# Optimization experiments

Measured on AMD Instinct MI355X. Metric: run time of the kernel, lower is better.

## Reference

```python
import jax, jax.numpy as jnp
import numpy as np

EPS = 1e-5

def conv(x, w, stride=1, pad=0, groups=1):
    # x: NCHW, w: OIHW
    return jax.lax.conv_general_dilated(
        x, w, window_strides=(stride, stride),
        padding=[(pad, pad), (pad, pad)],
        dimension_numbers=("NCHW", "OIHW", "NCHW"),
        feature_group_count=groups)

def bn_eval(x, gamma, beta, mean, var):
    scale = (gamma / jnp.sqrt(var + EPS))[None, :, None, None]
    shift = (beta - mean * gamma / jnp.sqrt(var + EPS))[None, :, None, None]
    return x * scale + shift

def setup_inputs() -> dict:
    key = jax.random.key(0)
    ks = jax.random.split(key, 12)
    B, Cin, H, W = 32, 64, 56, 56
    hidden, red, Cout, K = 384, 16, 64, 3
    f32 = jnp.float32
    x = jax.random.normal(ks[0], (B, Cin, H, W), dtype=f32)
    w_exp = jax.random.normal(ks[1], (hidden, Cin, 3, 3), dtype=f32) * 0.05
    w_dw  = jax.random.normal(ks[2], (hidden, 1, K, K), dtype=f32) * 0.1
    w_se1 = jax.random.normal(ks[3], (red, hidden, 1, 1), dtype=f32) * 0.05
    w_se2 = jax.random.normal(ks[4], (hidden, red, 1, 1), dtype=f32) * 0.1
    w_pw  = jax.random.normal(ks[5], (Cout, hidden, 1, 1), dtype=f32) * 0.05
    def bn_params(k, c):
        k1, k2 = jax.random.split(k)
        return (jnp.ones((c,), f32), jnp.zeros((c,), f32),
                jax.random.normal(k1, (c,), dtype=f32) * 0.01,
                jax.random.uniform(k2, (c,), dtype=f32, minval=0.5, maxval=1.5))
    g1, b1, m1, v1 = bn_params(ks[6], hidden)
    g2, b2, m2, v2 = bn_params(ks[7], hidden)
    g3, b3, m3, v3 = bn_params(ks[8], Cout)
    return dict(x=x, w_exp=w_exp, g1=g1, b1=b1, m1=m1, v1=v1,
                w_dw=w_dw, g2=g2, b2=b2, m2=m2, v2=v2,
                w_se1=w_se1, w_se2=w_se2, w_pw=w_pw,
                g3=g3, b3=b3, m3=m3, v3=v3)

def reference(x, w_exp, g1, b1, m1, v1, w_dw, g2, b2, m2, v2,
              w_se1, w_se2, w_pw, g3, b3, m3, v3):
    hidden = w_exp.shape[0]
    # expand conv (3x3) + BN + SiLU
    h = jax.nn.silu(bn_eval(conv(x, w_exp, stride=1, pad=1), g1, b1, m1, v1))
    # depthwise conv + BN + SiLU
    d = jax.nn.silu(bn_eval(conv(h, w_dw, stride=1, pad=1, groups=hidden), g2, b2, m2, v2))
    # squeeze-excitation: global avg pool -> 1x1 -> SiLU -> 1x1 -> sigmoid -> scale
    s = jnp.mean(d, axis=(2, 3), keepdims=True)            # [B, hidden, 1, 1]
    s = jax.nn.silu(conv(s, w_se1))
    s = jax.nn.sigmoid(conv(s, w_se2))
    d = d * s
    # pointwise projection + BN
    y = bn_eval(conv(d, w_pw), g3, b3, m3, v3)
    # eval mode: stochastic_depth is identity; quant_skip == (identity-quantized) input
    return y + x
```

## Files before the change

### kernel.cpp

```cpp
#include <hip/hip_runtime.h>

typedef unsigned short u16;
typedef unsigned int u32;
typedef __attribute__((ext_vector_type(2))) u32 u32x2;
typedef __attribute__((ext_vector_type(4))) u32 u32x4;
typedef __attribute__((ext_vector_type(4))) float f32x4;
typedef __attribute__((ext_vector_type(8))) short s16x8;

#define DEV __device__ __forceinline__

DEV float bflo(u32 u){ union{u32 i; float f;} c; c.i = u << 16; return c.f; }
DEV float bfhi(u32 u){ union{u32 i; float f;} c; c.i = u & 0xffff0000u; return c.f; }
DEV u16 f2b(float f){
  union{float f; u32 u;} c; c.f = f;
  u32 u = c.u;
  u32 r = (u + 0x7fffu + ((u >> 16) & 1u)) >> 16;
  return (u16)r;
}
DEV float fsilu(float v){ return v / (1.f + __expf(-v)); }

constexpr int Bn = 32, Cin = 64, H = 56, Wd = 56, HID = 384, CO = 64;
constexpr int HW = H * Wd;
constexpr float EPS = 1e-5f;

constexpr int XROW = 72 * 64;
constexpr int WTAP = 128 * 64;
constexpr int WOCT = 9 * WTAP;

__global__ __launch_bounds__(256) void k_prep_wbn(
    const float* __restrict__ w,
    const float* __restrict__ g1, const float* __restrict__ b1,
    const float* __restrict__ m1, const float* __restrict__ v1,
    const float* __restrict__ g3, const float* __restrict__ b3,
    const float* __restrict__ m3, const float* __restrict__ v3,
    u16* __restrict__ wt,
    float* __restrict__ sc1, float* __restrict__ sh1,
    float* __restrict__ sc3, float* __restrict__ sh3)
{
  const int blk = blockIdx.x;
  if (blk < 864) {
    int t = blk * 256 + threadIdx.x;
    int octile = t / WOCT, r = t - octile * WOCT;
    int tap = r / WTAP, r2 = r - tap * WTAP;
    int ocl = r2 >> 6, col = r2 & 63;
    int physo = col >> 3, j = col & 7;
    int olog = physo ^ (ocl & 7);
    int ic = olog * 8 + j;
    int oc = octile * 128 + ocl;
    wt[t] = f2b(w[(oc * Cin + ic) * 9 + tap]);
  } else {
    for (int t = threadIdx.x; t < HID; t += 256) {
      float sc = g1[t] * rsqrtf(v1[t] + EPS);
      sc1[t] = sc;
      sh1[t] = b1[t] - m1[t] * sc;
    }
    if (threadIdx.x < CO) {
      int t = threadIdx.x;
      float sc = g3[t] * rsqrtf(v3[t] + EPS);
      sc3[t] = sc;
      sh3[t] = b3[t] - m3[t] * sc;
    }
  }
}

__global__ __launch_bounds__(256, 2) void k_expand_mfma(
    const float* __restrict__ x, const u16* __restrict__ wt,
    const float* __restrict__ sc1, const float* __restrict__ sh1,
    u16* __restrict__ h, int b0)
{
  __shared__ u16 sB[4 * XROW];
  __shared__ u16 sA[2][WTAP];
  const int tid = threadIdx.x;
  const int ypair = blockIdx.x, b = blockIdx.y;
  const int gb = b0 + b;
  const int y0 = ypair * 2;
  const int wave = tid >> 6, ln = tid & 63;
  const int wm = wave >> 1, wn = wave & 1;
  const int lane15 = ln & 15, quad = ln >> 4;

  {
    u32x4 z = {0, 0, 0, 0};
    #pragma unroll
    for (int i = 0; i < 18; ++i)
      *(u32x4*)&sB[(i * 256 + tid) * 8] = z;
  }
  __syncthreads();
  {
    const int ic = tid & 63, xq = tid >> 6;
    #pragma unroll
    for (int r = 0; r < 4; ++r) {
      const int y = y0 + r - 1;
      if (y >= 0 && y < H) {
        const float* xp = x + ((size_t)(gb * Cin + ic) * H + y) * Wd + xq * 14;
        float vals[14];
        #pragma unroll
        for (int t = 0; t < 14; ++t) vals[t] = xp[t];
        u16* rowp = &sB[r * XROW];
        #pragma unroll
        for (int t = 0; t < 14; ++t) {
          int slot = xq * 14 + t + 1;
          int pos = slot * 64 + (((ic >> 3) ^ (slot & 7)) << 3) + (ic & 7);
          rowp[pos] = f2b(vals[t]);
        }
      }
    }
  }
  {
    #pragma unroll
    for (int it = 0; it < 4; ++it) {
      int i = it * 256 + tid;
      *(u32x4*)&sA[0][i * 8] = *(const u32x4*)&wt[i * 8];
    }
  }
  __syncthreads();

  const int y = y0 + wn;

  f32x4 acc[4][4];
  #pragma unroll
  for (int ms = 0; ms < 4; ++ms)
    #pragma unroll
    for (int ns = 0; ns < 4; ++ns) acc[ms][ns] = (f32x4){0.f, 0.f, 0.f, 0.f};

  int buf = 0;
  int octile = 0, tap = 0;
  for (int step = 0; step < 27; ++step) {
    u32x4 pf0, pf1, pf2, pf3;
    const bool pre = (step < 26);
    if (pre) {
      const u16* wnx = wt + (size_t)(step + 1) * WTAP;
      pf0 = *(const u32x4*)&wnx[(0 * 256 + tid) * 8];
      pf1 = *(const u32x4*)&wnx[(1 * 256 + tid) * 8];
      pf2 = *(const u32x4*)&wnx[(2 * 256 + tid) * 8];
      pf3 = *(const u32x4*)&wnx[(3 * 256 + tid) * 8];
    }

    const int dy = tap / 3, dx = tap - dy * 3;
    const u16* sAc = sA[buf];
    #pragma unroll
    for (int kk = 0; kk < 2; ++kk) {
      s16x8 af[4], bf[4];
      #pragma unroll
      for (int ms = 0; ms < 4; ++ms) {
        int ocl = wm * 64 + ms * 16 + lane15;
        int po = (kk * 4 + quad) ^ (ocl & 7);
        af[ms] = *(const s16x8*)&sAc[ocl * 64 + po * 8];
      }
      #pragma unroll
      for (int ns = 0; ns < 4; ++ns) {
        int row = wn + dy;
        int slot = ns * 16 + lane15 + dx;
        int po = (kk * 4 + quad) ^ (slot & 7);
        bf[ns] = *(const s16x8*)&sB[(row * 72 + slot) * 64 + po * 8];
      }
      #pragma unroll
      for (int ms = 0; ms < 4; ++ms)
        #pragma unroll
        for (int ns = 0; ns < 4; ++ns)
          acc[ms][ns] = __builtin_amdgcn_mfma_f32_16x16x32_bf16(
              af[ms], bf[ns], acc[ms][ns], 0, 0, 0);
    }

    if (pre) {
      u16* sAn = sA[buf ^ 1];
      *(u32x4*)&sAn[(0 * 256 + tid) * 8] = pf0;
      *(u32x4*)&sAn[(1 * 256 + tid) * 8] = pf1;
      *(u32x4*)&sAn[(2 * 256 + tid) * 8] = pf2;
      *(u32x4*)&sAn[(3 * 256 + tid) * 8] = pf3;
    }
    __syncthreads();
    buf ^= 1;

    if (++tap == 9) {
      #pragma unroll
      for (int ms = 0; ms < 4; ++ms) {
        int oc0 = octile * 128 + wm * 64 + ms * 16 + quad * 4;
        f32x4 sc = *(const f32x4*)&sc1[oc0];
        f32x4 sh = *(const f32x4*)&sh1[oc0];
        float scr[4] = {sc.x, sc.y, sc.z, sc.w};
        float shr[4] = {sh.x, sh.y, sh.z, sh.w};
        #pragma unroll
        for (int ns = 0; ns < 4; ++ns) {
          int xg = ns * 16 + lane15;
          if (xg < Wd) {
            float av[4] = {acc[ms][ns].x, acc[ms][ns].y, acc[ms][ns].z, acc[ms][ns].w};
            #pragma unroll
            for (int r = 0; r < 4; ++r) {
              float val = fsilu(av[r] * scr[r] + shr[r]);
              h[((size_t)(b * HID + oc0 + r) * H + y) * Wd + xg] = f2b(val);
            }
          }
        }
      }
      #pragma unroll
      for (int ms = 0; ms < 4; ++ms)
        #pragma unroll
        for (int ns = 0; ns < 4; ++ns) acc[ms][ns] = (f32x4){0.f, 0.f, 0.f, 0.f};
      tap = 0;
      ++octile;
    }
  }
}

__global__ __launch_bounds__(256) void k_dw(
    const u16* __restrict__ h, const float* __restrict__ wdw,
    const float* __restrict__ g2, const float* __restrict__ b2,
    const float* __restrict__ m2, const float* __restrict__ v2,
    u16* __restrict__ d, float* __restrict__ mean)
{
  __shared__ float red[4];
  const int tid = threadIdx.x;
  const int c = blockIdx.x, b = blockIdx.y;
  const u32* hp32 = (const u32*)(h + (size_t)(b * HID + c) * HW);

  float wv[9];
  #pragma unroll
  for (int t = 0; t < 9; ++t) wv[t] = wdw[c * 9 + t];
  const float sc = g2[c] * rsqrtf(v2[c] + EPS);
  const float sh = b2[c] - m2[c] * sc;

  float lsum = 0.f;
  if (tid < 224) {
    const int row = tid >> 2, seg = tid & 3;
    const int px0 = seg * 14, w0 = px0 >> 1;

    float v[3][16];
    #pragma unroll
    for (int r3 = 0; r3 < 3; ++r3) {
      int rr = row + r3 - 1;
      bool ok = (rr >= 0) && (rr < 56);
      const u32* rp = hp32 + rr * 28;
      v[r3][0] = (ok && seg > 0) ? bfhi(rp[w0 - 1]) : 0.f;
      #pragma unroll
      for (int t = 0; t < 7; ++t) {
        u32 wd = ok ? rp[w0 + t] : 0u;
        v[r3][1 + 2 * t] = bflo(wd);
        v[r3][2 + 2 * t] = bfhi(wd);
      }
      v[r3][15] = (ok && seg < 3) ? bflo(rp[w0 + 7]) : 0.f;
    }

    u32 pk[7];
    #pragma unroll
    for (int t = 0; t < 7; ++t) {
      float o2[2];
      #pragma unroll
      for (int e = 0; e < 2; ++e) {
        int j = 2 * t + e;
        float s = 0.f;
        #pragma unroll
        for (int r3 = 0; r3 < 3; ++r3)
          #pragma unroll
          for (int dx = 0; dx < 3; ++dx)
            s += v[r3][j + dx] * wv[r3 * 3 + dx];
        float val = fsilu(s * sc + sh);
        lsum += val;
        o2[e] = val;
      }
      pk[t] = (u32)f2b(o2[0]) | ((u32)f2b(o2[1]) << 16);
    }
    u32* dp32 = (u32*)(d + (size_t)(b * HID + c) * HW) + row * 28 + w0;
    #pragma unroll
    for (int t = 0; t < 7; ++t) dp32[t] = pk[t];
  }

  #pragma unroll
  for (int off = 32; off > 0; off >>= 1) lsum += __shfl_down(lsum, off);
  if ((tid & 63) == 0) red[tid >> 6] = lsum;
  __syncthreads();
  if (tid == 0)
    mean[b * HID + c] = (red[0] + red[1] + red[2] + red[3]) * (1.f / 3136.f);
}

__global__ __launch_bounds__(256) void k_se(
    const float* __restrict__ mean, const float* __restrict__ w1,
    const float* __restrict__ w2, float* __restrict__ sfac)
{
  __shared__ float sm[HID];
  __shared__ float ps[16 * 17];
  __shared__ float s1[16];
  const int b = blockIdx.x, tid = threadIdx.x;
  for (int c = tid; c < HID; c += 256) sm[c] = mean[b * HID + c];
  __syncthreads();
  int r = tid >> 4, j = tid & 15;
  float p = 0.f;
  for (int c = j; c < HID; c += 16) p += sm[c] * w1[r * HID + c];
  ps[r * 17 + j] = p;
  __syncthreads();
  if (tid < 16) {
    float s = 0.f;
    #pragma unroll
    for (int q = 0; q < 16; ++q) s += ps[tid * 17 + q];
    s1[tid] = fsilu(s);
  }
  __syncthreads();
  for (int c = tid; c < HID; c += 256) {
    float s = 0.f;
    #pragma unroll
    for (int q = 0; q < 16; ++q) s += s1[q] * w2[c * 16 + q];
    sfac[b * HID + c] = 1.f / (1.f + __expf(-s));
  }
}

constexpr int PWP = 392;

__global__ __launch_bounds__(256, 2) void k_pw_mfma(
    const u16* __restrict__ d, const float* __restrict__ sfac,
    const float* __restrict__ wpw,
    const float* __restrict__ sc3, const float* __restrict__ sh3,
    const float* __restrict__ x, float* __restrict__ out, int b0)
{
  __shared__ u16 sAw[64 * PWP];
  __shared__ u32 dtw[4 * 1024];
  const int tid = threadIdx.x;
  const int b = blockIdx.y, gb = b0 + b;
  const int p0 = blockIdx.x * 256;
  const int wave = tid >> 6, ln = tid & 63;
  const int lane15 = ln & 15, quad = ln >> 4;

  {
    for (int i = tid; i < 6144; i += 256) {
      int e = i * 4, co = e / 384, k = e - co * 384;
      f32x4 wv = *(const f32x4*)&wpw[e];
      f32x4 sf = *(const f32x4*)&sfac[b * HID + k];
      float s3 = sc3[co];
      u32x2 pk;
      pk.x = (u32)f2b(wv.x * sf.x * s3) | ((u32)f2b(wv.y * sf.y * s3) << 16);
      pk.y = (u32)f2b(wv.z * sf.z * s3) | ((u32)f2b(wv.w * sf.w * s3) << 16);
      *(u32x2*)&sAw[co * PWP + k] = pk;
    }
  }
  __syncthreads();

  f32x4 acc[4][4];
  #pragma unroll
  for (int ms = 0; ms < 4; ++ms)
    #pragma unroll
    for (int ns = 0; ns < 4; ++ns) acc[ms][ns] = (f32x4){0.f, 0.f, 0.f, 0.f};

  const int cpair8 = ln >> 3;
  const int pxo = (ln & 7) * 8;
  const int swz = ln & 3;
  const int pbase = p0 + wave * 64;
  u32* mydt = &dtw[wave * 1024];
  const bool ld_ok = (pbase + pxo + 8 <= HW);
  const u16* dbase = d + (size_t)b * HID * HW + pbase + pxo;

  u32x4 pr0[2], pr1[2];
  #pragma unroll
  for (int ci = 0; ci < 2; ++ci) {
    pr0[ci] = (u32x4){0,0,0,0}; pr1[ci] = (u32x4){0,0,0,0};
    if (ld_ok) {
      int c = 2 * (ci * 8 + cpair8);
      const u16* dpp = dbase + (size_t)c * HW;
      pr0[ci] = *(const u32x4*)dpp;
      pr1[ci] = *(const u32x4*)(dpp + HW);
    }
  }

  for (int ks = 0; ks < 12; ++ks) {
    #pragma unroll
    for (int ci = 0; ci < 2; ++ci) {
      int k4 = ci * 2 + (cpair8 >> 2);
      u32* w0 = &mydt[pxo * 16 + ((k4 ^ swz) << 2) + (cpair8 & 3)];
      u32x4 r0 = pr0[ci], r1 = pr1[ci];
      w0[0 * 16] = (r0.x & 0xffffu) | (r1.x << 16);
      w0[1 * 16] = (r0.x >> 16)     | (r1.x & 0xffff0000u);
      w0[2 * 16] = (r0.y & 0xffffu) | (r1.y << 16);
      w0[3 * 16] = (r0.y >> 16)     | (r1.y & 0xffff0000u);
      w0[4 * 16] = (r0.z & 0xffffu) | (r1.z << 16);
      w0[5 * 16] = (r0.z >> 16)     | (r1.z & 0xffff0000u);
      w0[6 * 16] = (r0.w & 0xffffu) | (r1.w << 16);
      w0[7 * 16] = (r0.w >> 16)     | (r1.w & 0xffff0000u);
    }
    if (ks < 11) {
      #pragma unroll
      for (int ci = 0; ci < 2; ++ci) {
        if (ld_ok) {
          int c = (ks + 1) * 32 + 2 * (ci * 8 + cpair8);
          const u16* dpp = dbase + (size_t)c * HW;
          pr0[ci] = *(const u32x4*)dpp;
          pr1[ci] = *(const u32x4*)(dpp + HW);
        }
      }
    }
    const int k0 = ks * 32;
    s16x8 af[4], bf[4];
    #pragma unroll
    for (int ms = 0; ms < 4; ++ms) {
      int ocl = ms * 16 + lane15;
      af[ms] = *(const s16x8*)&sAw[ocl * PWP + k0 + quad * 8];
    }
    #pragma unroll
    for (int ns = 0; ns < 4; ++ns) {
      int pxl = ns * 16 + lane15;
      int p4 = quad ^ ((pxl >> 3) & 3);
      bf[ns] = *(const s16x8*)((const u16*)mydt + pxl * 32 + p4 * 8);
    }
    #pragma unroll
    for (int ms = 0; ms < 4; ++ms)
      #pragma unroll
      for (int ns = 0; ns < 4; ++ns)
        acc[ms][ns] = __builtin_amdgcn_mfma_f32_16x16x32_bf16(
            af[ms], bf[ns], acc[ms][ns], 0, 0, 0);
  }

  #pragma unroll
  for (int ns = 0; ns < 4; ++ns) {
    int p = pbase + ns * 16 + lane15;
    if (p < HW) {
      #pragma unroll
      for (int ms = 0; ms < 4; ++ms) {
        int co0 = ms * 16 + quad * 4;
        float av[4] = {acc[ms][ns].x, acc[ms][ns].y, acc[ms][ns].z, acc[ms][ns].w};
        #pragma unroll
        for (int r = 0; r < 4; ++r) {
          size_t idx = (size_t)(gb * CO + co0 + r) * HW + p;
          out[idx] = av[r] + sh3[co0 + r] + x[idx];
        }
      }
    }
  }
}

extern "C" void kernel_launch(void* const* d_in, const int* in_sizes, int n_in,
                              void* d_out, int out_size, void* d_ws, size_t ws_size,
                              hipStream_t stream)
{
  (void)in_sizes; (void)n_in; (void)out_size;
  const float* x     = (const float*)d_in[0];
  const float* w_exp = (const float*)d_in[1];
  const float* g1 = (const float*)d_in[2];
  const float* b1 = (const float*)d_in[3];
  const float* m1 = (const float*)d_in[4];
  const float* v1 = (const float*)d_in[5];
  const float* w_dw = (const float*)d_in[6];
  const float* g2 = (const float*)d_in[7];
  const float* b2 = (const float*)d_in[8];
  const float* m2 = (const float*)d_in[9];
  const float* v2 = (const float*)d_in[10];
  const float* w_se1 = (const float*)d_in[11];
  const float* w_se2 = (const float*)d_in[12];
  const float* w_pw  = (const float*)d_in[13];
  const float* g3 = (const float*)d_in[14];
  const float* b3 = (const float*)d_in[15];
  const float* m3 = (const float*)d_in[16];
  const float* v3 = (const float*)d_in[17];

  const size_t perB = (size_t)HID * HW * 2 * 2 + HID * 8;
  const size_t fixed = 221184 * 2 + HID * 8 + CO * 8;
  int bc = Bn;
  while (bc > 1 && fixed + (size_t)bc * perB > ws_size) bc >>= 1;

  u16* wt = (u16*)d_ws;
  float* sc1 = (float*)(wt + 221184);
  float* sh1 = sc1 + HID;
  float* sc3 = sh1 + HID;
  float* sh3 = sc3 + CO;
  u16* h  = (u16*)(sh3 + CO);
  u16* dd = h + (size_t)bc * HID * HW;
  float* mean = (float*)(dd + (size_t)bc * HID * HW);
  float* sfac = mean + (size_t)bc * HID;

  k_prep_wbn<<<865, 256, 0, stream>>>(w_exp, g1, b1, m1, v1, g3, b3, m3, v3,
                                      wt, sc1, sh1, sc3, sh3);

  for (int b0 = 0; b0 < Bn; b0 += bc) {
    k_expand_mfma<<<dim3(28, bc), 256, 0, stream>>>(x, wt, sc1, sh1, h, b0);
    k_dw<<<dim3(HID, bc), 256, 0, stream>>>(h, w_dw, g2, b2, m2, v2, dd, mean);
    k_se<<<bc, 256, 0, stream>>>(mean, w_se1, w_se2, sfac);
    k_pw_mfma<<<dim3(13, bc), 256, 0, stream>>>(dd, sfac, w_pw, sc3, sh3,
                                                x, (float*)d_out, b0);
  }
}
```

Before: 263.0 us.

## Read expand-conv weights straight from global memory and fuse SE into pointwise kernel

The expand conv kernel drops its double-buffered LDS staging of weight taps and the per-step block barriers. Each lane now loads its A fragments directly from global memory through precomputed swizzled offsets, and the launch bound is raised to 3 blocks per CU because LDS use is smaller. The squeeze-excitation computation moves into the pointwise MFMA kernel, which removes one launch and the sfac buffer round trip. The cost is that each of the 13 pointwise blocks per image recomputes the SE MLP, and the expand kernel now depends on cache hits for uncoalesced weight loads with no prefetch.

New measurement: 389.7 us. 48.2% more time.

```diff
diff --git a/kernel.cpp b/kernel.cpp
--- a/kernel.cpp
+++ b/kernel.cpp
@@ -63,13 +63,12 @@
   }
 }
 
-__global__ __launch_bounds__(256, 2) void k_expand_mfma(
+__global__ __launch_bounds__(256, 3) void k_expand_mfma(
     const float* __restrict__ x, const u16* __restrict__ wt,
     const float* __restrict__ sc1, const float* __restrict__ sh1,
     u16* __restrict__ h, int b0)
 {
   __shared__ u16 sB[4 * XROW];
-  __shared__ u16 sA[2][WTAP];
   const int tid = threadIdx.x;
   const int ypair = blockIdx.x, b = blockIdx.y;
   const int gb = b0 + b;
@@ -81,7 +80,7 @@
   {
     u32x4 z = {0, 0, 0, 0};
     #pragma unroll
-    for (int i = 0; i < 18; ++i)
+    for (int i = 0; i < 9; ++i)
       *(u32x4*)&sB[(i * 256 + tid) * 8] = z;
   }
   __syncthreads();
@@ -105,99 +104,77 @@
       }
     }
   }
-  {
-    #pragma unroll
-    for (int it = 0; it < 4; ++it) {
-      int i = it * 256 + tid;
-      *(u32x4*)&sA[0][i * 8] = *(const u32x4*)&wt[i * 8];
-    }
-  }
   __syncthreads();
 
   const int y = y0 + wn;
 
-  f32x4 acc[4][4];
-  #pragma unroll
-  for (int ms = 0; ms < 4; ++ms)
-    #pragma unroll
-    for (int ns = 0; ns < 4; ++ns) acc[ms][ns] = (f32x4){0.f, 0.f, 0.f, 0.f};
-
-  int buf = 0;
-  int octile = 0, tap = 0;
-  for (int step = 0; step < 27; ++step) {
-    u32x4 pf0, pf1, pf2, pf3;
-    const bool pre = (step < 26);
-    if (pre) {
-      const u16* wnx = wt + (size_t)(step + 1) * WTAP;
-      pf0 = *(const u32x4*)&wnx[(0 * 256 + tid) * 8];
-      pf1 = *(const u32x4*)&wnx[(1 * 256 + tid) * 8];
-      pf2 = *(const u32x4*)&wnx[(2 * 256 + tid) * 8];
-      pf3 = *(const u32x4*)&wnx[(3 * 256 + tid) * 8];
-    }
-
-    const int dy = tap / 3, dx = tap - dy * 3;
-    const u16* sAc = sA[buf];
+  int woff[4][2];
+  #pragma unroll
+  for (int ms = 0; ms < 4; ++ms) {
+    int ocl = wm * 64 + ms * 16 + lane15;
     #pragma unroll
     for (int kk = 0; kk < 2; ++kk) {
-      s16x8 af[4], bf[4];
-      #pragma unroll
-      for (int ms = 0; ms < 4; ++ms) {
-        int ocl = wm * 64 + ms * 16 + lane15;
-        int po = (kk * 4 + quad) ^ (ocl & 7);
-        af[ms] = *(const s16x8*)&sAc[ocl * 64 + po * 8];
-      }
+      int po = (kk * 4 + quad) ^ (ocl & 7);
+      woff[ms][kk] = ocl * 64 + po * 8;
+    }
+  }
+
+  for (int octile = 0; octile < 3; ++octile) {
+    f32x4 acc[4][4];
+    #pragma unroll
+    for (int ms = 0; ms < 4; ++ms)
+      #pragma unroll
+      for (int ns = 0; ns < 4; ++ns) acc[ms][ns] = (f32x4){0.f, 0.f, 0.f, 0.f};
+
+    const u16* wsrc = wt + (size_t)octile * WOCT;
+    #pragma unroll
+    for (int tap = 0; tap < 9; ++tap) {
+      const int dy = tap / 3, dx = tap - dy * 3;
+      const u16* wtp = wsrc + tap * WTAP;
+      s16x8 af[4][2];
+      #pragma unroll
+      for (int ms = 0; ms < 4; ++ms)
+        #pragma unroll
+        for (int kk = 0; kk < 2; ++kk)
+          af[ms][kk] = *(const s16x8*)&wtp[woff[ms][kk]];
+      #pragma unroll
+      for (int kk = 0; kk < 2; ++kk) {
+        s16x8 bf[4];
+        #pragma unroll
+        for (int ns = 0; ns < 4; ++ns) {
+          int row = wn + dy;
+          int slot = ns * 16 + lane15 + dx;
+          int po = (kk * 4 + quad) ^ (slot & 7);
+          bf[ns] = *(const s16x8*)&sB[(row * 72 + slot) * 64 + po * 8];
+        }
+        #pragma unroll
+        for (int ms = 0; ms < 4; ++ms)
+          #pragma unroll
+          for (int ns = 0; ns < 4; ++ns)
+            acc[ms][ns] = __builtin_amdgcn_mfma_f32_16x16x32_bf16(
+                af[ms][kk], bf[ns], acc[ms][ns], 0, 0, 0);
+      }
+    }
+
+    #pragma unroll
+    for (int ms = 0; ms < 4; ++ms) {
+      int oc0 = octile * 128 + wm * 64 + ms * 16 + quad * 4;
+      f32x4 sc = *(const f32x4*)&sc1[oc0];
+      f32x4 sh = *(const f32x4*)&sh1[oc0];
+      float scr[4] = {sc.x, sc.y, sc.z, sc.w};
+      float shr[4] = {sh.x, sh.y, sh.z, sh.w};
       #pragma unroll
       for (int ns = 0; ns < 4; ++ns) {
-        int row = wn + dy;
-        int slot = ns * 16 + lane15 + dx;
-        int po = (kk * 4 + quad) ^ (slot & 7);
-        bf[ns] = *(const s16x8*)&sB[(row * 72 + slot) * 64 + po * 8];
-      }
-      #pragma unroll
-      for (int ms = 0; ms < 4; ++ms)
-        #pragma unroll
-        for (int ns = 0; ns < 4; ++ns)
-          acc[ms][ns] = __builtin_amdgcn_mfma_f32_16x16x32_bf16(
-              af[ms], bf[ns], acc[ms][ns], 0, 0, 0);
-    }
-
-    if (pre) {
-      u16* sAn = sA[buf ^ 1];
-      *(u32x4*)&sAn[(0 * 256 + tid) * 8] = pf0;
-      *(u32x4*)&sAn[(1 * 256 + tid) * 8] = pf1;
-      *(u32x4*)&sAn[(2 * 256 + tid) * 8] = pf2;
-      *(u32x4*)&sAn[(3 * 256 + tid) * 8] = pf3;
-    }
-    __syncthreads();
-    buf ^= 1;
-
-    if (++tap == 9) {
-      #pragma unroll
-      for (int ms = 0; ms < 4; ++ms) {
-        int oc0 = octile * 128 + wm * 64 + ms * 16 + quad * 4;
-        f32x4 sc = *(const f32x4*)&sc1[oc0];
-        f32x4 sh = *(const f32x4*)&sh1[oc0];
-        float scr[4] = {sc.x, sc.y, sc.z, sc.w};
-        float shr[4] = {sh.x, sh.y, sh.z, sh.w};
-        #pragma unroll
-        for (int ns = 0; ns < 4; ++ns) {
-          int xg = ns * 16 + lane15;
-          if (xg < Wd) {
-            float av[4] = {acc[ms][ns].x, acc[ms][ns].y, acc[ms][ns].z, acc[ms][ns].w};
-            #pragma unroll
-            for (int r = 0; r < 4; ++r) {
-              float val = fsilu(av[r] * scr[r] + shr[r]);
-              h[((size_t)(b * HID + oc0 + r) * H + y) * Wd + xg] = f2b(val);
-            }
+        int xg = ns * 16 + lane15;
+        if (xg < Wd) {
+          float av[4] = {acc[ms][ns].x, acc[ms][ns].y, acc[ms][ns].z, acc[ms][ns].w};
+          #pragma unroll
+          for (int r = 0; r < 4; ++r) {
+            float val = fsilu(av[r] * scr[r] + shr[r]);
+            h[((size_t)(b * HID + oc0 + r) * H + y) * Wd + xg] = f2b(val);
           }
         }
       }
-      #pragma unroll
-      for (int ms = 0; ms < 4; ++ms)
-        #pragma unroll
-        for (int ns = 0; ns < 4; ++ns) acc[ms][ns] = (f32x4){0.f, 0.f, 0.f, 0.f};
-      tap = 0;
-      ++octile;
     }
   }
 }
@@ -272,57 +249,56 @@
     mean[b * HID + c] = (red[0] + red[1] + red[2] + red[3]) * (1.f / 3136.f);
 }
 
-__global__ __launch_bounds__(256) void k_se(
-    const float* __restrict__ mean, const float* __restrict__ w1,
-    const float* __restrict__ w2, float* __restrict__ sfac)
-{
-  __shared__ float sm[HID];
-  __shared__ float ps[16 * 17];
-  __shared__ float s1[16];
-  const int b = blockIdx.x, tid = threadIdx.x;
-  for (int c = tid; c < HID; c += 256) sm[c] = mean[b * HID + c];
-  __syncthreads();
-  int r = tid >> 4, j = tid & 15;
-  float p = 0.f;
-  for (int c = j; c < HID; c += 16) p += sm[c] * w1[r * HID + c];
-  ps[r * 17 + j] = p;
-  __syncthreads();
-  if (tid < 16) {
-    float s = 0.f;
-    #pragma unroll
-    for (int q = 0; q < 16; ++q) s += ps[tid * 17 + q];
-    s1[tid] = fsilu(s);
-  }
-  __syncthreads();
-  for (int c = tid; c < HID; c += 256) {
-    float s = 0.f;
-    #pragma unroll
-    for (int q = 0; q < 16; ++q) s += s1[q] * w2[c * 16 + q];
-    sfac[b * HID + c] = 1.f / (1.f + __expf(-s));
-  }
-}
-
 constexpr int PWP = 392;
 
 __global__ __launch_bounds__(256, 2) void k_pw_mfma(
-    const u16* __restrict__ d, const float* __restrict__ sfac,
+    const u16* __restrict__ d, const float* __restrict__ mean,
+    const float* __restrict__ w1, const float* __restrict__ w2,
     const float* __restrict__ wpw,
     const float* __restrict__ sc3, const float* __restrict__ sh3,
     const float* __restrict__ x, float* __restrict__ out, int b0)
 {
   __shared__ u16 sAw[64 * PWP];
   __shared__ u32 dtw[4 * 1024];
+  __shared__ float smn[HID];
+  __shared__ float sps[16 * 17];
+  __shared__ float ss1[16];
+  __shared__ float ssf[HID];
   const int tid = threadIdx.x;
   const int b = blockIdx.y, gb = b0 + b;
   const int p0 = blockIdx.x * 256;
   const int wave = tid >> 6, ln = tid & 63;
   const int lane15 = ln & 15, quad = ln >> 4;
 
+  for (int c = tid; c < HID; c += 256) smn[c] = mean[b * HID + c];
+  __syncthreads();
+  {
+    int r = tid >> 4, j = tid & 15;
+    float p = 0.f;
+    for (int c = j; c < HID; c += 16) p += smn[c] * w1[r * HID + c];
+    sps[r * 17 + j] = p;
+  }
+  __syncthreads();
+  if (tid < 16) {
+    float s = 0.f;
+    #pragma unroll
+    for (int q = 0; q < 16; ++q) s += sps[tid * 17 + q];
+    ss1[tid] = fsilu(s);
+  }
+  __syncthreads();
+  for (int c = tid; c < HID; c += 256) {
+    float s = 0.f;
+    #pragma unroll
+    for (int q = 0; q < 16; ++q) s += ss1[q] * w2[c * 16 + q];
+    ssf[c] = 1.f / (1.f + __expf(-s));
+  }
+  __syncthreads();
+
   {
     for (int i = tid; i < 6144; i += 256) {
       int e = i * 4, co = e / 384, k = e - co * 384;
       f32x4 wv = *(const f32x4*)&wpw[e];
-      f32x4 sf = *(const f32x4*)&sfac[b * HID + k];
+      f32x4 sf = *(const f32x4*)&ssf[k];
       float s3 = sc3[co];
       u32x2 pk;
       pk.x = (u32)f2b(wv.x * sf.x * s3) | ((u32)f2b(wv.y * sf.y * s3) << 16);
@@ -460,7 +436,6 @@
   u16* h  = (u16*)(sh3 + CO);
   u16* dd = h + (size_t)bc * HID * HW;
   float* mean = (float*)(dd + (size_t)bc * HID * HW);
-  float* sfac = mean + (size_t)bc * HID;
 
   k_prep_wbn<<<865, 256, 0, stream>>>(w_exp, g1, b1, m1, v1, g3, b3, m3, v3,
                                       wt, sc1, sh1, sc3, sh3);
@@ -468,8 +443,7 @@
   for (int b0 = 0; b0 < Bn; b0 += bc) {
     k_expand_mfma<<<dim3(28, bc), 256, 0, stream>>>(x, wt, sc1, sh1, h, b0);
     k_dw<<<dim3(HID, bc), 256, 0, stream>>>(h, w_dw, g2, b2, m2, v2, dd, mean);
-    k_se<<<bc, 256, 0, stream>>>(mean, w_se1, w_se2, sfac);
-    k_pw_mfma<<<dim3(13, bc), 256, 0, stream>>>(dd, sfac, w_pw, sc3, sh3,
-                                                x, (float*)d_out, b0);
-  }
-}
+    k_pw_mfma<<<dim3(13, bc), 256, 0, stream>>>(dd, mean, w_se1, w_se2, w_pw,
+                                                sc3, sh3, x, (float*)d_out, b0);
+  }
+}
```
